# Optimization experiments

Hardware: AMD Instinct MI355X
Metric: run time of the kernel (lower is better)

Reference implementation:

```python
import jax, jax.numpy as jnp
import numpy as np

ORDER = 256
THETA = 23.0
HIDDEN = 512
INPUT_DIM = 256
BATCH = 8192
TIMESTEPS = 23
LEAKY_SLOPE = 0.2  # tf.nn.leaky_relu default alpha


def _expm_np(M):
    # scaling-and-squaring + Taylor series, float64 numpy (replaces scipy expm)
    n = M.shape[0]
    nrm = np.linalg.norm(M, 1)
    s = max(0, int(np.ceil(np.log2(max(nrm, 1e-30)))) + 1)
    Ms = M / (2.0 ** s)
    E = np.eye(n)
    term = np.eye(n)
    for k in range(1, 30):
        term = term @ Ms / k
        E = E + term
    for _ in range(s):
        E = E @ E
    return E


def get_state_space_matrices(order, theta):
    Q = np.arange(order, dtype=np.float64)
    R = (2 * Q + 1)[:, None] / theta
    j, i = np.meshgrid(Q, Q)
    A = np.where(i < j, -1, (-1.0) ** (i - j + 1)) * R
    B = (-1.0) ** Q[:, None] * R
    # zero-order-hold discretization with dt=1: expm of augmented matrix
    aug = np.zeros((order + 1, order + 1))
    aug[:order, :order] = A
    aug[:order, order:] = B
    M = _expm_np(aug)
    return M[:order, :order], M[:order, order:]


def setup_inputs() -> dict:
    key = jax.random.key(0)
    ks = jax.random.split(key, 5)
    A_np, B_np = get_state_space_matrices(ORDER, THETA)

    def glorot(k, shape):
        lim = np.sqrt(6.0 / (shape[0] + shape[1]))
        return jax.random.uniform(k, shape, jnp.float32, -lim, lim)

    return {
        "inputs": jax.random.normal(ks[0], (BATCH, TIMESTEPS, INPUT_DIM), jnp.float32),
        "A": jnp.asarray(A_np, jnp.float32),          # [order, order]
        "B": jnp.asarray(B_np, jnp.float32),          # [order, 1]
        "W_h": glorot(ks[1], (HIDDEN, HIDDEN)),
        "W_m": glorot(ks[2], (HIDDEN, ORDER)),
        "W_x": glorot(ks[3], (INPUT_DIM, HIDDEN)),
        "e_x": glorot(ks[4], (INPUT_DIM, 1)),
    }


def reference(inputs, A, B, W_h, W_m, W_x, e_x):
    batch = inputs.shape[0]
    Bv = B[:, 0]  # [order]

    def step(carry, x_t):  # x_t: [batch, input_dim]
        h, m = carry  # h: [batch, hidden], m: [batch, order]
        u = x_t @ e_x  # [batch, 1]
        m_new = m @ A.T + u * Bv[None, :]          # [batch, order]
        pre = x_t @ W_x + h @ W_h.T + m_new @ W_m.T  # [batch, hidden]
        h_new = jnp.where(pre >= 0, pre, LEAKY_SLOPE * pre)
        return (h_new, m_new), h_new

    h0 = jnp.zeros((batch, W_h.shape[0]), inputs.dtype)
    m0 = jnp.zeros((batch, A.shape[0]), inputs.dtype)
    xs = jnp.transpose(inputs, (1, 0, 2))  # [T, batch, input_dim]
    _, hs = jax.lax.scan(step, (h0, m0), xs)
    return jnp.transpose(hs, (1, 0, 2))  # [batch, T, hidden]
```

## Files before the change

kernel.cpp:

```cpp
#include <hip/hip_runtime.h>

#define T_STEPS 23
#define ORD 256
#define HID 512
#define IN_DIM 256
#define NBATCH 8192
#define SLOPE 0.2f
#define LDH (T_STEPS * HID)

__device__ __forceinline__ float lrelu(float x) { return x >= 0.f ? x : SLOPE * x; }

__device__ __forceinline__ ushort f2bf(float x) {
    unsigned u = __float_as_uint(x);
    u += 0x7fffu + ((u >> 16) & 1u);
    return (ushort)(u >> 16);
}
__device__ __forceinline__ float bf2f(ushort h) { return __uint_as_float((unsigned)h << 16); }

typedef __attribute__((ext_vector_type(8))) short bf16x8;
typedef __attribute__((ext_vector_type(4))) float f32x4;

__global__ void vchain_kernel(const float* __restrict__ A,
                              const float* __restrict__ Bv,
                              float* __restrict__ V) {
    __shared__ float v[ORD];
    int i = threadIdx.x;
    v[i] = Bv[i];
    __syncthreads();
    for (int k = 0; k < T_STEPS; ++k) {
        V[k * ORD + i] = v[i];
        float a = 0.f;
        const float4* ar = (const float4*)(A + i * ORD);
        const float4* vr = (const float4*)v;
        #pragma unroll 8
        for (int t = 0; t < ORD / 4; ++t) {
            float4 a4 = ar[t];
            float4 v4 = vr[t];
            a += a4.x * v4.x + a4.y * v4.y + a4.z * v4.z + a4.w * v4.w;
        }
        __syncthreads();
        v[i] = a;
        __syncthreads();
    }
}

__global__ void wtab_kernel(const float* __restrict__ Wm,
                            const float* __restrict__ V,
                            float* __restrict__ wtab) {
    __shared__ float vs[ORD];
    int k = blockIdx.x;
    int j = blockIdx.y * 64 + threadIdx.x;
    ((float4*)vs)[threadIdx.x] = ((const float4*)(V + k * ORD))[threadIdx.x];
    __syncthreads();
    float a = 0.f;
    const float4* wr = (const float4*)(Wm + j * ORD);
    const float4* vr = (const float4*)vs;
    #pragma unroll 8
    for (int i = 0; i < ORD / 4; ++i) {
        float4 w4 = wr[i];
        float4 v4 = vr[i];
        a += w4.x * v4.x + w4.y * v4.y + w4.z * v4.z + w4.w * v4.w;
    }
    wtab[k * HID + j] = a;
}

__global__ void u_kernel(const float* __restrict__ X,
                         const float* __restrict__ ex,
                         float* __restrict__ u) {
    int row = blockIdx.x * 4 + (threadIdx.x >> 6);
    int lane = threadIdx.x & 63;
    const float4* xp = (const float4*)(X + (size_t)row * IN_DIM);
    const float4* ep = (const float4*)ex;
    float4 x4 = xp[lane];
    float4 e4 = ep[lane];
    float acc = x4.x * e4.x + x4.y * e4.y + x4.z * e4.z + x4.w * e4.w;
    #pragma unroll
    for (int off = 32; off; off >>= 1) acc += __shfl_down(acc, off);
    if (lane == 0) u[row] = acc;
}

__global__ __launch_bounds__(256) void gemm_xwx(const float* __restrict__ X,
                                                const float* __restrict__ Wx,
                                                float* __restrict__ out) {
    __shared__ float As[16][68];
    __shared__ float Bs[16][68];
    int tid = threadIdx.x;
    int row0 = blockIdx.x * 64;
    int col0 = blockIdx.y * 64;
    int tx = tid & 15, ty = tid >> 4;
    int am = tid >> 2, ak4 = tid & 3;
    float acc[4][4] = {};
    for (int k0 = 0; k0 < 256; k0 += 16) {
        float4 av = *(const float4*)(X + (size_t)(row0 + am) * IN_DIM + k0 + ak4 * 4);
        float4 bv = *(const float4*)(Wx + (size_t)(k0 + ty) * HID + col0 + tx * 4);
        __syncthreads();
        As[ak4 * 4 + 0][am] = av.x;
        As[ak4 * 4 + 1][am] = av.y;
        As[ak4 * 4 + 2][am] = av.z;
        As[ak4 * 4 + 3][am] = av.w;
        *(float4*)&Bs[ty][tx * 4] = bv;
        __syncthreads();
        #pragma unroll
        for (int kk = 0; kk < 16; ++kk) {
            float4 a4 = *(const float4*)&As[kk][ty * 4];
            float4 b4 = *(const float4*)&Bs[kk][tx * 4];
            float a[4] = {a4.x, a4.y, a4.z, a4.w};
            float b[4] = {b4.x, b4.y, b4.z, b4.w};
            #pragma unroll
            for (int i = 0; i < 4; ++i)
                #pragma unroll
                for (int j = 0; j < 4; ++j)
                    acc[i][j] += a[i] * b[j];
        }
    }
    #pragma unroll
    for (int i = 0; i < 4; ++i) {
        float4 v = make_float4(acc[i][0], acc[i][1], acc[i][2], acc[i][3]);
        *(float4*)(out + (size_t)(row0 + ty * 4 + i) * HID + col0 + tx * 4) = v;
    }
}

__global__ __launch_bounds__(512) void memconv_kernel(const float* __restrict__ u,
                                                      const float* __restrict__ wtab,
                                                      float* __restrict__ out) {
    int b = blockIdx.x, j = threadIdx.x;
    __shared__ float us[T_STEPS];
    if (j < T_STEPS) us[j] = u[b * T_STEPS + j];
    float w[T_STEPS];
    #pragma unroll
    for (int k = 0; k < T_STEPS; ++k) w[k] = wtab[k * HID + j];
    __syncthreads();
    float* ob = out + (size_t)b * LDH + j;
    #pragma unroll
    for (int t = 0; t < T_STEPS; ++t) {
        float acc = 0.f;
        #pragma unroll
        for (int s = 0; s <= t; ++s) acc += us[s] * w[t - s];
        ob[t * HID] += acc;
    }
}

__global__ void whpack_kernel(const float* __restrict__ Wh,
                              ushort* __restrict__ whi,
                              ushort* __restrict__ wlo) {
    int f = blockIdx.x;
    int s = blockIdx.y;
    int l = threadIdx.x;
    int n = f * 16 + (l & 15);
    int k0 = s * 32 + 4 * (l >> 4);
    float4 a = *(const float4*)(Wh + (size_t)n * HID + k0);
    float4 b = *(const float4*)(Wh + (size_t)n * HID + k0 + 16);
    float v[8] = {a.x, a.y, a.z, a.w, b.x, b.y, b.z, b.w};
    unsigned hp[4], lp[4];
    #pragma unroll
    for (int e2 = 0; e2 < 4; ++e2) {
        ushort h0 = f2bf(v[2 * e2]),     h1 = f2bf(v[2 * e2 + 1]);
        ushort l0 = f2bf(v[2 * e2]     - bf2f(h0));
        ushort l1 = f2bf(v[2 * e2 + 1] - bf2f(h1));
        hp[e2] = (unsigned)h0 | ((unsigned)h1 << 16);
        lp[e2] = (unsigned)l0 | ((unsigned)l1 << 16);
    }
    size_t off = ((size_t)(f * 16 + s) * 64 + l) * 8;
    *(uint4*)(whi + off) = make_uint4(hp[0], hp[1], hp[2], hp[3]);
    *(uint4*)(wlo + off) = make_uint4(lp[0], lp[1], lp[2], lp[3]);
}


__device__ __forceinline__ bf16x8 ld_frag(const ushort* base, int o1, int o2) {
    ushort4 p = *(const ushort4*)(base + o1);
    ushort4 q = *(const ushort4*)(base + o2);
    bf16x8 r;
    r[0] = (short)p.x; r[1] = (short)p.y; r[2] = (short)p.z; r[3] = (short)p.w;
    r[4] = (short)q.x; r[5] = (short)q.y; r[6] = (short)q.z; r[7] = (short)q.w;
    return r;
}

__device__ __forceinline__ void store_hilo(ushort* hhi, ushort* hlo, int off, float4 v) {
    ushort h0 = f2bf(v.x), h1 = f2bf(v.y), h2 = f2bf(v.z), h3 = f2bf(v.w);
    *(ushort4*)(hhi + off) = make_ushort4(h0, h1, h2, h3);
    ushort l0 = f2bf(v.x - bf2f(h0));
    ushort l1 = f2bf(v.y - bf2f(h1));
    ushort l2 = f2bf(v.z - bf2f(h2));
    ushort l3 = f2bf(v.w - bf2f(h3));
    *(ushort4*)(hlo + off) = make_ushort4(l0, l1, l2, l3);
}

__global__ __launch_bounds__(512) void rec_fused(const ushort* __restrict__ whi,
                                                 const ushort* __restrict__ wlo,
                                                 float* __restrict__ out) {
    __shared__ ushort hhi[32 * 512];
    __shared__ ushort hlo[32 * 512];
    const int tid = threadIdx.x;
    const int w  = tid >> 6;
    const int l  = tid & 63;
    const int lm = l & 15;
    const int g  = l >> 4;
    const int row0 = blockIdx.x * 32;
    const int xsw = lm << 2;

    float* obase[2];
    obase[0] = out + (size_t)(row0 + lm) * LDH + w * 64 + 4 * g;
    obase[1] = out + (size_t)(row0 + 16 + lm) * LDH + w * 64 + 4 * g;

    #pragma unroll
    for (int bi = 0; bi < 2; ++bi) {
        #pragma unroll
        for (int jf = 0; jf < 4; ++jf) {
            float4 vv = *(float4*)(obase[bi] + jf * 16);
            vv.x = lrelu(vv.x); vv.y = lrelu(vv.y); vv.z = lrelu(vv.z); vv.w = lrelu(vv.w);
            *(float4*)(obase[bi] + jf * 16) = vv;
            int m  = bi * 16 + lm;
            int nb = w * 64 + jf * 16 + 4 * g;
            store_hilo(hhi, hlo, m * 512 + (nb ^ xsw), vv);
        }
    }

    const ushort* wh_l = whi + (size_t)w * 32768 + (size_t)l * 8;
    const ushort* wl_l = wlo + (size_t)w * 32768 + (size_t)l * 8;

    #pragma unroll 1
    for (int t = 1; t < T_STEPS; ++t) {
        __syncthreads();

        f32x4 acc[4][2];
        #pragma unroll
        for (int jf = 0; jf < 4; ++jf)
            #pragma unroll
            for (int bi = 0; bi < 2; ++bi) {
                float4 p = *(float4*)(obase[bi] + t * HID + jf * 16);
                acc[jf][bi][0] = p.x; acc[jf][bi][1] = p.y;
                acc[jf][bi][2] = p.z; acc[jf][bi][3] = p.w;
            }

        #pragma unroll
        for (int s = 0; s < 16; ++s) {
            bf16x8 ah[4], al[4], bh[2], bl[2];
            #pragma unroll
            for (int jf = 0; jf < 4; ++jf) {
                ah[jf] = *(const bf16x8*)(wh_l + jf * 8192 + s * 512);
                al[jf] = *(const bf16x8*)(wl_l + jf * 8192 + s * 512);
            }
            #pragma unroll
            for (int bi = 0; bi < 2; ++bi) {
                int m  = bi * 16 + lm;
                int o1 = m * 512 + ((s * 32 + 4 * g)      ^ xsw);
                int o2 = m * 512 + ((s * 32 + 16 + 4 * g) ^ xsw);
                bh[bi] = ld_frag(hhi, o1, o2);
                bl[bi] = ld_frag(hlo, o1, o2);
            }
            #pragma unroll
            for (int jf = 0; jf < 4; ++jf)
                #pragma unroll
                for (int bi = 0; bi < 2; ++bi) {
                    acc[jf][bi] = __builtin_amdgcn_mfma_f32_16x16x32_bf16(ah[jf], bh[bi], acc[jf][bi], 0, 0, 0);
                    acc[jf][bi] = __builtin_amdgcn_mfma_f32_16x16x32_bf16(ah[jf], bl[bi], acc[jf][bi], 0, 0, 0);
                    acc[jf][bi] = __builtin_amdgcn_mfma_f32_16x16x32_bf16(al[jf], bh[bi], acc[jf][bi], 0, 0, 0);
                }
        }

        __syncthreads();

        #pragma unroll
        for (int jf = 0; jf < 4; ++jf)
            #pragma unroll
            for (int bi = 0; bi < 2; ++bi) {
                float4 r;
                r.x = lrelu(acc[jf][bi][0]); r.y = lrelu(acc[jf][bi][1]);
                r.z = lrelu(acc[jf][bi][2]); r.w = lrelu(acc[jf][bi][3]);
                *(float4*)(obase[bi] + t * HID + jf * 16) = r;
                int m  = bi * 16 + lm;
                int nb = w * 64 + jf * 16 + 4 * g;
                store_hilo(hhi, hlo, m * 512 + (nb ^ xsw), r);
            }
    }
}

extern "C" void kernel_launch(void* const* d_in, const int* in_sizes, int n_in,
                              void* d_out, int out_size, void* d_ws, size_t ws_size,
                              hipStream_t stream) {
    const float* X  = (const float*)d_in[0];
    const float* A  = (const float*)d_in[1];
    const float* Bv = (const float*)d_in[2];
    const float* Wh = (const float*)d_in[3];
    const float* Wm = (const float*)d_in[4];
    const float* Wx = (const float*)d_in[5];
    const float* ex = (const float*)d_in[6];
    float* out = (float*)d_out;

    float* u    = (float*)d_ws;
    float* V    = u + NBATCH * T_STEPS;
    float* wtab = V + T_STEPS * ORD;
    ushort* whp_hi = (ushort*)(wtab + T_STEPS * HID);
    ushort* whp_lo = whp_hi + HID * HID;

    const int nrows = NBATCH * T_STEPS;

    vchain_kernel<<<1, 256, 0, stream>>>(A, Bv, V);
    wtab_kernel<<<dim3(T_STEPS, HID / 64), 64, 0, stream>>>(Wm, V, wtab);
    whpack_kernel<<<dim3(HID / 16, HID / 32), 64, 0, stream>>>(Wh, whp_hi, whp_lo);

    u_kernel<<<nrows / 4, 256, 0, stream>>>(X, ex, u);

    gemm_xwx<<<dim3(nrows / 64, HID / 64), 256, 0, stream>>>(X, Wx, out);

    memconv_kernel<<<NBATCH, HID, 0, stream>>>(u, wtab, out);

    rec_fused<<<NBATCH / 32, 512, 0, stream>>>(whp_hi, whp_lo, out);
}
```

Baseline: 2.402 ms.

## Double-buffer hidden state in LDS and split recurrent work across 16 waves

The recurrent kernel now runs 1024 threads per block, with each wave owning 32 output columns instead of 64. The bf16 hi/lo hidden-state copies in LDS are double-buffered, which removes one barrier per timestep. Each timestep's precomputed input projection is loaded into registers before the barrier and added after the MFMA loop, so the global-load latency overlaps the matmul. Output loads and stores use nontemporal hints. The costs are doubled LDS use (128KB) and more waves sharing each CU, which raises register pressure under the 1024-thread launch bound.

After: 2.591 ms. 1.08x slower.

```diff
diff --git a/kernel.cpp b/kernel.cpp
--- a/kernel.cpp
+++ b/kernel.cpp
@@ -7,6 +7,7 @@
 #define NBATCH 8192
 #define SLOPE 0.2f
 #define LDH (T_STEPS * HID)
+#define ROWS 32
 
 __device__ __forceinline__ float lrelu(float x) { return x >= 0.f ? x : SLOPE * x; }
 
@@ -19,6 +20,13 @@
 
 typedef __attribute__((ext_vector_type(8))) short bf16x8;
 typedef __attribute__((ext_vector_type(4))) float f32x4;
+
+__device__ __forceinline__ f32x4 nt_load4(const float* p) {
+    return __builtin_nontemporal_load((const f32x4*)p);
+}
+__device__ __forceinline__ void nt_store4(float* p, f32x4 v) {
+    __builtin_nontemporal_store(v, (f32x4*)p);
+}
 
 __global__ void vchain_kernel(const float* __restrict__ A,
                               const float* __restrict__ Bv,
@@ -175,68 +183,70 @@
     return r;
 }
 
-__device__ __forceinline__ void store_hilo(ushort* hhi, ushort* hlo, int off, float4 v) {
-    ushort h0 = f2bf(v.x), h1 = f2bf(v.y), h2 = f2bf(v.z), h3 = f2bf(v.w);
+__device__ __forceinline__ void store_hilo(ushort* hhi, ushort* hlo, int off, f32x4 v) {
+    ushort h0 = f2bf(v[0]), h1 = f2bf(v[1]), h2 = f2bf(v[2]), h3 = f2bf(v[3]);
     *(ushort4*)(hhi + off) = make_ushort4(h0, h1, h2, h3);
-    ushort l0 = f2bf(v.x - bf2f(h0));
-    ushort l1 = f2bf(v.y - bf2f(h1));
-    ushort l2 = f2bf(v.z - bf2f(h2));
-    ushort l3 = f2bf(v.w - bf2f(h3));
+    ushort l0 = f2bf(v[0] - bf2f(h0));
+    ushort l1 = f2bf(v[1] - bf2f(h1));
+    ushort l2 = f2bf(v[2] - bf2f(h2));
+    ushort l3 = f2bf(v[3] - bf2f(h3));
     *(ushort4*)(hlo + off) = make_ushort4(l0, l1, l2, l3);
 }
 
-__global__ __launch_bounds__(512) void rec_fused(const ushort* __restrict__ whi,
-                                                 const ushort* __restrict__ wlo,
-                                                 float* __restrict__ out) {
-    __shared__ ushort hhi[32 * 512];
-    __shared__ ushort hlo[32 * 512];
+__global__ __launch_bounds__(1024) void rec_fused(const ushort* __restrict__ whi,
+                                                  const ushort* __restrict__ wlo,
+                                                  float* __restrict__ out) {
+    __shared__ ushort hbuf[2][2][ROWS * 512];
     const int tid = threadIdx.x;
     const int w  = tid >> 6;
     const int l  = tid & 63;
     const int lm = l & 15;
     const int g  = l >> 4;
-    const int row0 = blockIdx.x * 32;
+    const int row0 = blockIdx.x * ROWS;
     const int xsw = lm << 2;
 
     float* obase[2];
-    obase[0] = out + (size_t)(row0 + lm) * LDH + w * 64 + 4 * g;
-    obase[1] = out + (size_t)(row0 + 16 + lm) * LDH + w * 64 + 4 * g;
+    obase[0] = out + (size_t)(row0 + lm) * LDH + w * 32 + 4 * g;
+    obase[1] = out + (size_t)(row0 + 16 + lm) * LDH + w * 32 + 4 * g;
 
     #pragma unroll
     for (int bi = 0; bi < 2; ++bi) {
         #pragma unroll
-        for (int jf = 0; jf < 4; ++jf) {
-            float4 vv = *(float4*)(obase[bi] + jf * 16);
-            vv.x = lrelu(vv.x); vv.y = lrelu(vv.y); vv.z = lrelu(vv.z); vv.w = lrelu(vv.w);
-            *(float4*)(obase[bi] + jf * 16) = vv;
+        for (int jf = 0; jf < 2; ++jf) {
+            f32x4 vv = nt_load4(obase[bi] + jf * 16);
+            vv[0] = lrelu(vv[0]); vv[1] = lrelu(vv[1]);
+            vv[2] = lrelu(vv[2]); vv[3] = lrelu(vv[3]);
+            nt_store4(obase[bi] + jf * 16, vv);
             int m  = bi * 16 + lm;
-            int nb = w * 64 + jf * 16 + 4 * g;
-            store_hilo(hhi, hlo, m * 512 + (nb ^ xsw), vv);
+            int nb = w * 32 + jf * 16 + 4 * g;
+            store_hilo(&hbuf[0][0][0], &hbuf[0][1][0], m * 512 + (nb ^ xsw), vv);
         }
     }
 
-    const ushort* wh_l = whi + (size_t)w * 32768 + (size_t)l * 8;
-    const ushort* wl_l = wlo + (size_t)w * 32768 + (size_t)l * 8;
-
+    const ushort* wh_l = whi + (size_t)w * 16384 + (size_t)l * 8;
+    const ushort* wl_l = wlo + (size_t)w * 16384 + (size_t)l * 8;
+
+    int buf = 0;
     #pragma unroll 1
     for (int t = 1; t < T_STEPS; ++t) {
-        __syncthreads();
-
-        f32x4 acc[4][2];
-        #pragma unroll
-        for (int jf = 0; jf < 4; ++jf)
-            #pragma unroll
-            for (int bi = 0; bi < 2; ++bi) {
-                float4 p = *(float4*)(obase[bi] + t * HID + jf * 16);
-                acc[jf][bi][0] = p.x; acc[jf][bi][1] = p.y;
-                acc[jf][bi][2] = p.z; acc[jf][bi][3] = p.w;
-            }
+        f32x4 pregs[2][2];
+        #pragma unroll
+        for (int jf = 0; jf < 2; ++jf)
+            #pragma unroll
+            for (int bi = 0; bi < 2; ++bi)
+                pregs[jf][bi] = nt_load4(obase[bi] + t * HID + jf * 16);
+
+        __syncthreads();
+
+        const ushort* hh = &hbuf[buf][0][0];
+        const ushort* hl = &hbuf[buf][1][0];
+        f32x4 acc[2][2] = {};
 
         #pragma unroll
         for (int s = 0; s < 16; ++s) {
-            bf16x8 ah[4], al[4], bh[2], bl[2];
-            #pragma unroll
-            for (int jf = 0; jf < 4; ++jf) {
+            bf16x8 ah[2], al[2], bh[2], bl[2];
+            #pragma unroll
+            for (int jf = 0; jf < 2; ++jf) {
                 ah[jf] = *(const bf16x8*)(wh_l + jf * 8192 + s * 512);
                 al[jf] = *(const bf16x8*)(wl_l + jf * 8192 + s * 512);
             }
@@ -245,11 +255,11 @@
                 int m  = bi * 16 + lm;
                 int o1 = m * 512 + ((s * 32 + 4 * g)      ^ xsw);
                 int o2 = m * 512 + ((s * 32 + 16 + 4 * g) ^ xsw);
-                bh[bi] = ld_frag(hhi, o1, o2);
-                bl[bi] = ld_frag(hlo, o1, o2);
+                bh[bi] = ld_frag(hh, o1, o2);
+                bl[bi] = ld_frag(hl, o1, o2);
             }
             #pragma unroll
-            for (int jf = 0; jf < 4; ++jf)
+            for (int jf = 0; jf < 2; ++jf)
                 #pragma unroll
                 for (int bi = 0; bi < 2; ++bi) {
                     acc[jf][bi] = __builtin_amdgcn_mfma_f32_16x16x32_bf16(ah[jf], bh[bi], acc[jf][bi], 0, 0, 0);
@@ -258,19 +268,20 @@
                 }
         }
 
-        __syncthreads();
-
-        #pragma unroll
-        for (int jf = 0; jf < 4; ++jf)
+        buf ^= 1;
+        #pragma unroll
+        for (int jf = 0; jf < 2; ++jf)
             #pragma unroll
             for (int bi = 0; bi < 2; ++bi) {
-                float4 r;
-                r.x = lrelu(acc[jf][bi][0]); r.y = lrelu(acc[jf][bi][1]);
-                r.z = lrelu(acc[jf][bi][2]); r.w = lrelu(acc[jf][bi][3]);
-                *(float4*)(obase[bi] + t * HID + jf * 16) = r;
+                f32x4 r;
+                r[0] = lrelu(acc[jf][bi][0] + pregs[jf][bi][0]);
+                r[1] = lrelu(acc[jf][bi][1] + pregs[jf][bi][1]);
+                r[2] = lrelu(acc[jf][bi][2] + pregs[jf][bi][2]);
+                r[3] = lrelu(acc[jf][bi][3] + pregs[jf][bi][3]);
+                nt_store4(obase[bi] + t * HID + jf * 16, r);
                 int m  = bi * 16 + lm;
-                int nb = w * 64 + jf * 16 + 4 * g;
-                store_hilo(hhi, hlo, m * 512 + (nb ^ xsw), r);
+                int nb = w * 32 + jf * 16 + 4 * g;
+                store_hilo(&hbuf[buf][0][0], &hbuf[buf][1][0], m * 512 + (nb ^ xsw), r);
             }
     }
 }
@@ -305,5 +316,5 @@
 
     memconv_kernel<<<NBATCH, HID, 0, stream>>>(u, wtab, out);
 
-    rec_fused<<<NBATCH / 32, 512, 0, stream>>>(whp_hi, whp_lo, out);
-}
+    rec_fused<<<NBATCH / ROWS, 1024, 0, stream>>>(whp_hi, whp_lo, out);
+}
```
